# Kernel tuning notes

Hardware: AMD Instinct MI355X
Metric: run time of the kernel (lower is better)

The kernel has to match this reference:

```python
import jax, jax.numpy as jnp
import numpy as np

B, NQ, C = 2, 16384, 768
NH, NL, NP = 6, 1, 4
HW = 128
D = C // NH  # 128, deform_ratio = 1.0
EPS = 1e-6


def layernorm(x, g, b):
    m = jnp.mean(x, -1, keepdims=True)
    v = jnp.var(x, -1, keepdims=True)
    return (x - m) * jax.lax.rsqrt(v + EPS) * g + b


def setup_inputs() -> dict:
    key = jax.random.key(0)
    ks = jax.random.split(key, 16)
    n = lambda k, s, sc=1.0: jax.random.normal(k, s, jnp.float32) * sc
    return {
        "query": n(ks[0], (B, NQ, C)),
        "reference_points": jax.random.uniform(ks[1], (B, NQ, NL, 2), jnp.float32),
        "feat": n(ks[2], (B, NQ, C)),
        "spatial_shapes": jnp.array([[HW, HW]], jnp.int32),
        "level_start_index": jnp.array([0], jnp.int32),
        "qn_g": jnp.ones((C,), jnp.float32), "qn_b": jnp.zeros((C,), jnp.float32),
        "fn_g": jnp.ones((C,), jnp.float32), "fn_b": jnp.zeros((C,), jnp.float32),
        "gamma": n(ks[3], (C,), 0.1),
        "W_off": n(ks[4], (C, NH * NL * NP * 2), 0.02), "b_off": n(ks[5], (NH * NL * NP * 2,), 0.5),
        "W_attn": n(ks[6], (C, NH * NL * NP), 0.02), "b_attn": jnp.zeros((NH * NL * NP,), jnp.float32),
        "W_val": n(ks[7], (C, NH * D), 0.02), "b_val": jnp.zeros((NH * D,), jnp.float32),
        "W_out": n(ks[8], (NH * D, C), 0.02), "b_out": jnp.zeros((C,), jnp.float32),
    }


def _ms_deform_attn(q, rp, f, W_off, b_off, W_attn, b_attn, W_val, b_val, W_out, b_out, shapes, starts):
    Bq, Nq, _ = q.shape
    value = (f @ W_val + b_val).reshape(Bq, -1, NH, D)  # (B, Lin, H, D)
    off = (q @ W_off + b_off).reshape(Bq, Nq, NH, NL, NP, 2)
    aw = jax.nn.softmax((q @ W_attn + b_attn).reshape(Bq, Nq, NH, NL * NP), -1)
    aw = aw.reshape(Bq, Nq, NH, NL, NP)
    shapes_f = jnp.asarray(shapes, q.dtype)
    normalizer = jnp.stack([shapes_f[:, 1], shapes_f[:, 0]], -1)  # (NL, 2) = (W, H)
    loc = rp[:, :, None, :, None, :] + off / normalizer[None, None, None, :, None, :]
    out = jnp.zeros((Bq, Nq, NH, D), q.dtype)
    b_idx = jnp.arange(Bq)[:, None, None, None]
    h_idx = jnp.arange(NH)[None, None, :, None]
    for l in range(NL):
        Hl, Wl = int(shapes[l, 0]), int(shapes[l, 1])
        s = int(starts[l])
        v = value[:, s:s + Hl * Wl].reshape(Bq, Hl, Wl, NH, D)
        ll = loc[:, :, :, l]                        # (B, Nq, H, P, 2)
        # grid_sample bilinear, align_corners=False, zero padding
        x = ll[..., 0] * Wl - 0.5
        y = ll[..., 1] * Hl - 0.5
        x0 = jnp.floor(x); y0 = jnp.floor(y)
        x1 = x0 + 1.0;     y1 = y0 + 1.0
        wx1 = x - x0; wx0 = 1.0 - wx1
        wy1 = y - y0; wy0 = 1.0 - wy1
        def corner(xi, yi, w):
            valid = (xi >= 0) & (xi <= Wl - 1) & (yi >= 0) & (yi <= Hl - 1)
            xc = jnp.clip(xi, 0, Wl - 1).astype(jnp.int32)
            yc = jnp.clip(yi, 0, Hl - 1).astype(jnp.int32)
            g = v[b_idx, yc, xc, h_idx]             # (B, Nq, H, P, D)
            return g * (w * valid)[..., None]
        samp = (corner(x0, y0, wx0 * wy0) + corner(x1, y0, wx1 * wy0)
                + corner(x0, y1, wx0 * wy1) + corner(x1, y1, wx1 * wy1))
        out = out + jnp.einsum('bqhpd,bqhp->bqhd', samp, aw[:, :, :, l])
    return out.reshape(Bq, Nq, NH * D) @ W_out + b_out


def reference(query, reference_points, feat, spatial_shapes, level_start_index,
              qn_g, qn_b, fn_g, fn_b, gamma,
              W_off, b_off, W_attn, b_attn, W_val, b_val, W_out, b_out):
    shapes = np.asarray(spatial_shapes)
    starts = np.asarray(level_start_index)
    q = layernorm(query, qn_g, qn_b)
    f = layernorm(feat, fn_g, fn_b)
    attn = _ms_deform_attn(q, reference_points, f, W_off, b_off, W_attn, b_attn,
                           W_val, b_val, W_out, b_out, shapes, starts)
    return query + gamma * attn
```

## Files before the change

kernel.cpp:

```cpp
#include <hip/hip_runtime.h>
#include <stdint.h>

typedef unsigned short u16;
typedef float f32x4 __attribute__((ext_vector_type(4)));
typedef short s16x8 __attribute__((ext_vector_type(8)));

#define K_DIM 768
#define M_ROWS 32768
#define NQ_ 16384
#define HW_ 128

__device__ __forceinline__ float bf2f(u16 u) {
    union { uint32_t u; float f; } c; c.u = ((uint32_t)u) << 16; return c.f;
}
__device__ __forceinline__ u16 f2bf(float f) {
    union { float f; uint32_t u; } c; c.f = f;
    uint32_t u = c.u;
    u += 0x7FFFu + ((u >> 16) & 1);
    return (u16)(u >> 16);
}

__device__ __forceinline__ void gload_lds16(const void* g, void* l) {
    __builtin_amdgcn_global_load_lds((const __attribute__((address_space(1))) void*)g,
                                     (__attribute__((address_space(3))) void*)l, 16, 0, 0);
}

__global__ void prep_wt_kernel(const float* __restrict__ W, u16* __restrict__ Wt, int Ncols) {
    int idx = blockIdx.x * 256 + threadIdx.x;
    if (idx >= Ncols * K_DIM) return;
    int n = idx / K_DIM, k = idx - n * K_DIM;
    Wt[idx] = f2bf(W[(size_t)k * Ncols + n]);
}

__global__ void prep_woa_kernel(const float* __restrict__ Woff, const float* __restrict__ Wattn,
                                const float* __restrict__ boff, const float* __restrict__ battn,
                                u16* __restrict__ Wt, float* __restrict__ bias) {
    int idx = blockIdx.x * 256 + threadIdx.x;
    if (idx >= 128 * K_DIM) return;
    int n = idx / K_DIM, k = idx - n * K_DIM;
    float v = 0.0f;
    if (n < 48)      v = Woff[(size_t)k * 48 + n];
    else if (n < 72) v = Wattn[(size_t)k * 24 + (n - 48)];
    Wt[idx] = f2bf(v);
    if (idx < 128) bias[idx] = idx < 48 ? boff[idx] : (idx < 72 ? battn[idx - 48] : 0.0f);
}

__global__ __launch_bounds__(192) void ln_kernel(const float* __restrict__ x,
                                                 const float* __restrict__ g,
                                                 const float* __restrict__ b,
                                                 u16* __restrict__ out) {
    int row = blockIdx.x;
    int tid = threadIdx.x;
    const float4 v = ((const float4*)(x + (size_t)row * K_DIM))[tid];
    float s  = v.x + v.y + v.z + v.w;
    float s2 = v.x * v.x + v.y * v.y + v.z * v.z + v.w * v.w;
#pragma unroll
    for (int off = 32; off >= 1; off >>= 1) {
        s  += __shfl_down(s, off);
        s2 += __shfl_down(s2, off);
    }
    __shared__ float red[6];
    int wv = tid >> 6, lane = tid & 63;
    if (lane == 0) { red[wv] = s; red[3 + wv] = s2; }
    __syncthreads();
    s  = red[0] + red[1] + red[2];
    s2 = red[3] + red[4] + red[5];
    float mean = s * (1.0f / K_DIM);
    float var  = s2 * (1.0f / K_DIM) - mean * mean;
    float inv  = rsqrtf(var + 1e-6f);
    const float4 gg = ((const float4*)g)[tid];
    const float4 bb = ((const float4*)b)[tid];
    ushort4 o;
    o.x = f2bf((v.x - mean) * inv * gg.x + bb.x);
    o.y = f2bf((v.y - mean) * inv * gg.y + bb.y);
    o.z = f2bf((v.z - mean) * inv * gg.z + bb.z);
    o.w = f2bf((v.w - mean) * inv * gg.w + bb.w);
    ((ushort4*)(out + (size_t)row * K_DIM))[tid] = o;
}

#define EP_BF16 0
#define EP_F32 1
#define EP_FINAL 2

template <int EP, int NX, int BN = 128>
__global__ __launch_bounds__(256) void gemm_kernel(
        const u16* __restrict__ A, const u16* __restrict__ Bt,
        const float* __restrict__ bias, void* __restrict__ out, int ld_out,
        const float* __restrict__ query, const float* __restrict__ gamma) {
    constexpr int NF = BN / 32;
    constexpr int BUF = 16384 + BN * 128;
    constexpr int NWG = NX * (M_ROWS / 128);
    constexpr int CPX = NWG / 8;
    __shared__ __align__(16) char smem[2 * BUF];
    const int lane = threadIdx.x & 63;
    const int wv = threadIdx.x >> 6;
    const int wr = wv >> 1, wc = wv & 1;
    const int lr = lane & 15, lg = lane >> 4;
    const int wg  = blockIdx.x;
    const int swz = (wg & 7) * CPX + (wg >> 3);
    const int m0 = (swz / NX) * 128;
    const int n0 = (swz % NX) * BN;

    f32x4 acc[4][NF] = {};

    const u16* Ab = A + (size_t)m0 * K_DIM;
    const u16* Bb = Bt + (size_t)n0 * K_DIM;

    auto stage = [&](char* buf, int kt) {
#pragma unroll
        for (int c = 0; c < 4; ++c) {
            int chunk = wv * 4 + c;
            int row = chunk * 8 + (lane >> 3);
            int slot = (lane & 7) ^ (row & 7);
            gload_lds16(Ab + (size_t)row * K_DIM + kt + slot * 8, buf + chunk * 1024);
        }
#pragma unroll
        for (int c = 0; c < NF; ++c) {
            int chunk = wv * NF + c;
            int row = chunk * 8 + (lane >> 3);
            int slot = (lane & 7) ^ (row & 7);
            gload_lds16(Bb + (size_t)row * K_DIM + kt + slot * 8, buf + 16384 + chunk * 1024);
        }
    };

    stage(smem, 0);
    asm volatile("s_waitcnt vmcnt(0)" ::: "memory");
    __builtin_amdgcn_s_barrier();
    __builtin_amdgcn_sched_barrier(0);

    constexpr int NT = K_DIM / 64;
    int cur = 0;
#pragma unroll 2
    for (int t = 0; t < NT; ++t) {
        const char* rb = smem + cur * BUF;
        if (t + 1 < NT) stage(smem + (cur ^ 1) * BUF, (t + 1) * 64);
#pragma unroll
        for (int kk = 0; kk < 2; ++kk) {
            s16x8 af[4], bfr[NF];
#pragma unroll
            for (int m = 0; m < 4; ++m) {
                int row = wr * 64 + m * 16 + lr;
                int slot = (kk * 4 + lg) ^ (row & 7);
                af[m] = *(const s16x8*)(rb + row * 128 + slot * 16);
            }
#pragma unroll
            for (int n = 0; n < NF; ++n) {
                int row = wc * (BN / 2) + n * 16 + lr;
                int slot = (kk * 4 + lg) ^ (row & 7);
                bfr[n] = *(const s16x8*)(rb + 16384 + row * 128 + slot * 16);
            }
            __builtin_amdgcn_s_setprio(1);
#pragma unroll
            for (int m = 0; m < 4; ++m)
#pragma unroll
                for (int n = 0; n < NF; ++n)
                    acc[m][n] = __builtin_amdgcn_mfma_f32_16x16x32_bf16(af[m], bfr[n], acc[m][n], 0, 0, 0);
            __builtin_amdgcn_s_setprio(0);
        }
        asm volatile("s_waitcnt vmcnt(0)" ::: "memory");
        __builtin_amdgcn_s_barrier();
        __builtin_amdgcn_sched_barrier(0);
        cur ^= 1;
    }

#pragma unroll
    for (int m = 0; m < 4; ++m) {
#pragma unroll
        for (int r = 0; r < 4; ++r) {
            int row = m0 + wr * 64 + m * 16 + lg * 4 + r;
#pragma unroll
            for (int n = 0; n < NF; ++n) {
                int col = n0 + wc * (BN / 2) + n * 16 + lr;
                float v = acc[m][n][r] + bias[col];
                if constexpr (EP == EP_BF16) {
                    ((u16*)out)[(size_t)row * ld_out + col] = f2bf(v);
                } else if constexpr (EP == EP_F32) {
                    if (col < 72)
                        ((float*)out)[(size_t)row * ld_out + col] = v;
                } else {
                    size_t idx = (size_t)row * ld_out + col;
                    ((float*)out)[idx] = query[idx] + gamma[col] * v;
                }
            }
        }
    }
}

__global__ __launch_bounds__(384) void sample_kernel(
        const float* __restrict__ oa,
        const float* __restrict__ rp,
        const u16* __restrict__ value,
        u16* __restrict__ samp) {
    const int q = blockIdx.x;
    const int h = __builtin_amdgcn_readfirstlane(threadIdx.x >> 6);
    const int lane = threadIdx.x & 63;
    const int b = q >> 14;
    const float* oar = oa + (size_t)q * 128;

    const int p  = (lane >> 2) & 3;
    const int cn = lane & 3;
    const float lp = oar[48 + h * 4 + p];
    const float e  = __expf(lp);
    float es = e;
    es += __shfl_xor(es, 4);
    es += __shfl_xor(es, 8);
    const float aw = e * __builtin_amdgcn_rcpf(es);

    const float2 offv = *(const float2*)(oar + h * 8 + p * 2);
    const float2 rpv  = *(const float2*)(rp + (size_t)q * 2);
    const float xx = rpv.x * 128.0f + offv.x - 0.5f;
    const float yy = rpv.y * 128.0f + offv.y - 0.5f;
    const float x0 = floorf(xx), y0 = floorf(yy);
    const float fx = xx - x0, fy = yy - y0;
    const float cx = x0 + (float)(cn & 1);
    const float cy = y0 + (float)(cn >> 1);
    const float wx = (cn & 1) ? fx : 1.0f - fx;
    const float wy = (cn >> 1) ? fy : 1.0f - fy;
    const bool valid = (cx >= 0.0f) & (cx <= 127.0f) & (cy >= 0.0f) & (cy <= 127.0f);
    const float w = valid ? aw * wx * wy : 0.0f;
    const int cxi = (int)fminf(fmaxf(cx, 0.0f), 127.0f);
    const int cyi = (int)fminf(fmaxf(cy, 0.0f), 127.0f);
    const int ofs = (cyi * HW_ + cxi) * (K_DIM * 2);

    const char* vbs = (const char*)value + 2u * ((size_t)b * NQ_ * K_DIM + (size_t)h * 128);
    const int wbits = __float_as_int(w);
    float acc0 = 0.0f, acc1 = 0.0f;
#pragma unroll
    for (int c = 0; c < 16; ++c) {
        const float wc = __int_as_float(__builtin_amdgcn_readlane(wbits, c));
        const int   oc = __builtin_amdgcn_readlane(ofs, c);
        const uint32_t d = ((const uint32_t*)(vbs + oc))[lane];
        acc0 = fmaf(wc, __int_as_float(d << 16), acc0);
        acc1 = fmaf(wc, __int_as_float(d & 0xffff0000u), acc1);
    }
    ushort2 o; o.x = f2bf(acc0); o.y = f2bf(acc1);
    ((ushort2*)(samp + (size_t)q * K_DIM + h * 128))[lane] = o;
}

extern "C" void kernel_launch(void* const* d_in, const int* in_sizes, int n_in,
                              void* d_out, int out_size, void* d_ws, size_t ws_size,
                              hipStream_t stream) {
    (void)in_sizes; (void)n_in; (void)out_size; (void)ws_size;
    const float* query  = (const float*)d_in[0];
    const float* rp     = (const float*)d_in[1];
    const float* feat   = (const float*)d_in[2];
    const float* qn_g   = (const float*)d_in[5];
    const float* qn_b   = (const float*)d_in[6];
    const float* fn_g   = (const float*)d_in[7];
    const float* fn_b   = (const float*)d_in[8];
    const float* gamma  = (const float*)d_in[9];
    const float* W_off  = (const float*)d_in[10];
    const float* b_off  = (const float*)d_in[11];
    const float* W_attn = (const float*)d_in[12];
    const float* b_attn = (const float*)d_in[13];
    const float* W_val  = (const float*)d_in[14];
    const float* b_val  = (const float*)d_in[15];
    const float* W_out  = (const float*)d_in[16];
    const float* b_out  = (const float*)d_in[17];

    char* ws = (char*)d_ws;
    u16*   ln_buf  = (u16*)  (ws + 0);
    u16*   val_buf = (u16*)  (ws + 50331648);
    float* oa_buf  = (float*)(ws + 100663296);
    u16*   wv_t    = (u16*)  (ws + 117440512);
    u16*   wo_t    = (u16*)  (ws + 118620160);
    u16*   woa_t   = (u16*)  (ws + 119799808);
    float* bias_oa = (float*)(ws + 119996416);
    u16*   samp_buf = ln_buf;

    prep_wt_kernel<<<(768 * 768 + 255) / 256, 256, 0, stream>>>(W_val, wv_t, 768);
    prep_wt_kernel<<<(768 * 768 + 255) / 256, 256, 0, stream>>>(W_out, wo_t, 768);
    prep_woa_kernel<<<(128 * 768 + 255) / 256, 256, 0, stream>>>(W_off, W_attn, b_off, b_attn, woa_t, bias_oa);

    ln_kernel<<<M_ROWS, 192, 0, stream>>>(feat, fn_g, fn_b, ln_buf);

    gemm_kernel<EP_BF16, 6><<<6 * (M_ROWS / 128), 256, 0, stream>>>(ln_buf, wv_t, b_val, val_buf, 768, nullptr, nullptr);

    ln_kernel<<<M_ROWS, 192, 0, stream>>>(query, qn_g, qn_b, ln_buf);

    gemm_kernel<EP_F32, 2, 64><<<2 * (M_ROWS / 128), 256, 0, stream>>>(ln_buf, woa_t, bias_oa, oa_buf, 128, nullptr, nullptr);

    sample_kernel<<<M_ROWS, 384, 0, stream>>>(oa_buf, rp, val_buf, samp_buf);

    gemm_kernel<EP_FINAL, 6><<<6 * (M_ROWS / 128), 256, 0, stream>>>(samp_buf, wo_t, b_out, d_out, 768, query, gamma);
}
```

Measured before the change: 273.2 us.

## Use 8-wave GEMM workgroups and merge weight-prep kernels into one launch

The GEMM kernel now runs 512 threads per block, with the 8 waves laid out 2x4, so each wave computes a 64xBN/4 sub-tile. Global-to-LDS staging is split across the 8 waves. The aim is more resident waves to hide memory and LDS latency. In exchange each wave holds fewer accumulators and gets less MFMA reuse per fragment load, which raises LDS read traffic per FLOP. Separately, the three weight transpose/convert kernels are fused into a single launch to cut launch overhead.

```diff
diff --git a/kernel.cpp b/kernel.cpp
--- a/kernel.cpp
+++ b/kernel.cpp
@@ -25,24 +25,29 @@
                                      (__attribute__((address_space(3))) void*)l, 16, 0, 0);
 }
 
-__global__ void prep_wt_kernel(const float* __restrict__ W, u16* __restrict__ Wt, int Ncols) {
+__global__ void prep_all_kernel(const float* __restrict__ Wval, const float* __restrict__ Wout,
+                                const float* __restrict__ Woff, const float* __restrict__ Wattn,
+                                const float* __restrict__ boff, const float* __restrict__ battn,
+                                u16* __restrict__ wv_t, u16* __restrict__ wo_t,
+                                u16* __restrict__ woa_t, float* __restrict__ bias) {
     int idx = blockIdx.x * 256 + threadIdx.x;
-    if (idx >= Ncols * K_DIM) return;
-    int n = idx / K_DIM, k = idx - n * K_DIM;
-    Wt[idx] = f2bf(W[(size_t)k * Ncols + n]);
-}
-
-__global__ void prep_woa_kernel(const float* __restrict__ Woff, const float* __restrict__ Wattn,
-                                const float* __restrict__ boff, const float* __restrict__ battn,
-                                u16* __restrict__ Wt, float* __restrict__ bias) {
-    int idx = blockIdx.x * 256 + threadIdx.x;
-    if (idx >= 128 * K_DIM) return;
-    int n = idx / K_DIM, k = idx - n * K_DIM;
-    float v = 0.0f;
-    if (n < 48)      v = Woff[(size_t)k * 48 + n];
-    else if (n < 72) v = Wattn[(size_t)k * 24 + (n - 48)];
-    Wt[idx] = f2bf(v);
-    if (idx < 128) bias[idx] = idx < 48 ? boff[idx] : (idx < 72 ? battn[idx - 48] : 0.0f);
+    const int SZ = 768 * K_DIM;
+    if (idx < SZ) {
+        int n = idx / K_DIM, k = idx - n * K_DIM;
+        wv_t[idx] = f2bf(Wval[(size_t)k * 768 + n]);
+    } else if (idx < 2 * SZ) {
+        int r = idx - SZ;
+        int n = r / K_DIM, k = r - n * K_DIM;
+        wo_t[r] = f2bf(Wout[(size_t)k * 768 + n]);
+    } else if (idx < 2 * SZ + 128 * K_DIM) {
+        int r = idx - 2 * SZ;
+        int n = r / K_DIM, k = r - n * K_DIM;
+        float v = 0.0f;
+        if (n < 48)      v = Woff[(size_t)k * 48 + n];
+        else if (n < 72) v = Wattn[(size_t)k * 24 + (n - 48)];
+        woa_t[r] = f2bf(v);
+        if (r < 128) bias[r] = r < 48 ? boff[r] : (r < 72 ? battn[r - 48] : 0.0f);
+    }
 }
 
 __global__ __launch_bounds__(192) void ln_kernel(const float* __restrict__ x,
@@ -83,18 +88,19 @@
 #define EP_FINAL 2
 
 template <int EP, int NX, int BN = 128>
-__global__ __launch_bounds__(256) void gemm_kernel(
+__global__ __launch_bounds__(512) void gemm_kernel(
         const u16* __restrict__ A, const u16* __restrict__ Bt,
         const float* __restrict__ bias, void* __restrict__ out, int ld_out,
         const float* __restrict__ query, const float* __restrict__ gamma) {
-    constexpr int NF = BN / 32;
+    constexpr int NF = BN / 64;
+    constexpr int BCH = BN / 64;
     constexpr int BUF = 16384 + BN * 128;
     constexpr int NWG = NX * (M_ROWS / 128);
     constexpr int CPX = NWG / 8;
     __shared__ __align__(16) char smem[2 * BUF];
     const int lane = threadIdx.x & 63;
     const int wv = threadIdx.x >> 6;
-    const int wr = wv >> 1, wc = wv & 1;
+    const int wr = wv >> 2, wc = wv & 3;
     const int lr = lane & 15, lg = lane >> 4;
     const int wg  = blockIdx.x;
     const int swz = (wg & 7) * CPX + (wg >> 3);
@@ -108,15 +114,15 @@
 
     auto stage = [&](char* buf, int kt) {
 #pragma unroll
-        for (int c = 0; c < 4; ++c) {
-            int chunk = wv * 4 + c;
+        for (int c = 0; c < 2; ++c) {
+            int chunk = wv * 2 + c;
             int row = chunk * 8 + (lane >> 3);
             int slot = (lane & 7) ^ (row & 7);
             gload_lds16(Ab + (size_t)row * K_DIM + kt + slot * 8, buf + chunk * 1024);
         }
 #pragma unroll
-        for (int c = 0; c < NF; ++c) {
-            int chunk = wv * NF + c;
+        for (int c = 0; c < BCH; ++c) {
+            int chunk = wv * BCH + c;
             int row = chunk * 8 + (lane >> 3);
             int slot = (lane & 7) ^ (row & 7);
             gload_lds16(Bb + (size_t)row * K_DIM + kt + slot * 8, buf + 16384 + chunk * 1024);
@@ -145,7 +151,7 @@
             }
 #pragma unroll
             for (int n = 0; n < NF; ++n) {
-                int row = wc * (BN / 2) + n * 16 + lr;
+                int row = wc * (BN / 4) + n * 16 + lr;
                 int slot = (kk * 4 + lg) ^ (row & 7);
                 bfr[n] = *(const s16x8*)(rb + 16384 + row * 128 + slot * 16);
             }
@@ -170,7 +176,7 @@
             int row = m0 + wr * 64 + m * 16 + lg * 4 + r;
 #pragma unroll
             for (int n = 0; n < NF; ++n) {
-                int col = n0 + wc * (BN / 2) + n * 16 + lr;
+                int col = n0 + wc * (BN / 4) + n * 16 + lr;
                 float v = acc[m][n][r] + bias[col];
                 if constexpr (EP == EP_BF16) {
                     ((u16*)out)[(size_t)row * ld_out + col] = f2bf(v);
@@ -268,19 +274,18 @@
     float* bias_oa = (float*)(ws + 119996416);
     u16*   samp_buf = ln_buf;
 
-    prep_wt_kernel<<<(768 * 768 + 255) / 256, 256, 0, stream>>>(W_val, wv_t, 768);
-    prep_wt_kernel<<<(768 * 768 + 255) / 256, 256, 0, stream>>>(W_out, wo_t, 768);
-    prep_woa_kernel<<<(128 * 768 + 255) / 256, 256, 0, stream>>>(W_off, W_attn, b_off, b_attn, woa_t, bias_oa);
+    prep_all_kernel<<<(2 * 768 * 768 + 128 * 768 + 255) / 256, 256, 0, stream>>>(
+        W_val, W_out, W_off, W_attn, b_off, b_attn, wv_t, wo_t, woa_t, bias_oa);
 
     ln_kernel<<<M_ROWS, 192, 0, stream>>>(feat, fn_g, fn_b, ln_buf);
 
-    gemm_kernel<EP_BF16, 6><<<6 * (M_ROWS / 128), 256, 0, stream>>>(ln_buf, wv_t, b_val, val_buf, 768, nullptr, nullptr);
+    gemm_kernel<EP_BF16, 6><<<6 * (M_ROWS / 128), 512, 0, stream>>>(ln_buf, wv_t, b_val, val_buf, 768, nullptr, nullptr);
 
     ln_kernel<<<M_ROWS, 192, 0, stream>>>(query, qn_g, qn_b, ln_buf);
 
-    gemm_kernel<EP_F32, 2, 64><<<2 * (M_ROWS / 128), 256, 0, stream>>>(ln_buf, woa_t, bias_oa, oa_buf, 128, nullptr, nullptr);
+    gemm_kernel<EP_F32, 2, 64><<<2 * (M_ROWS / 128), 512, 0, stream>>>(ln_buf, woa_t, bias_oa, oa_buf, 128, nullptr, nullptr);
 
     sample_kernel<<<M_ROWS, 384, 0, stream>>>(oa_buf, rp, val_buf, samp_buf);
 
-    gemm_kernel<EP_FINAL, 6><<<6 * (M_ROWS / 128), 256, 0, stream>>>(samp_buf, wo_t, b_out, d_out, 768, query, gamma);
-}
+    gemm_kernel<EP_FINAL, 6><<<6 * (M_ROWS / 128), 512, 0, stream>>>(samp_buf, wo_t, b_out, d_out, 768, query, gamma);
+}
```

Result: faster. 258.7 us (-5.3%).
